# Optimization experiments

Measured on AMD Instinct MI355X. Metric: run time of the kernel, lower is better.

The kernel has to match this reference:

```python
import jax, jax.numpy as jnp
import numpy as np

B, N, D, K, V = 32, 4096, 256, 32, 16


def setup_inputs() -> dict:
    keys = jax.random.split(jax.random.key(0), 6)
    return {
        "rec_scalar_feats": jax.random.normal(keys[0], (B * N, D), jnp.float32),
        "rec_pos": jax.random.normal(keys[1], (B * N, 3), jnp.float32) * 10.0,
        "W_src": jax.random.normal(keys[2], (D, D), jnp.float32) * 0.05,   # nn.Linear weight [out,in]
        "W_dst": jax.random.normal(keys[3], (D, D), jnp.float32) * 0.05,
        "W_kp": jax.random.normal(keys[4], (D * K, D), jnp.float32) * 0.05,  # keypoint_embedding Linear
        "b_kp": jax.random.normal(keys[5], (D * K,), jnp.float32) * 0.01,
        "ln_gamma": jnp.ones((D * K,), jnp.float32),
        "ln_beta": jnp.zeros((D * K,), jnp.float32),
        "batch_size": B,
        "vector_size": V,
    }


def reference(rec_scalar_feats, rec_pos, W_src, W_dst, W_kp, b_kp, ln_gamma, ln_beta, batch_size, vector_size):
    d = rec_scalar_feats.shape[-1]
    b = batch_size
    n = rec_scalar_feats.shape[0] // b
    k = W_kp.shape[0] // d
    h = rec_scalar_feats.reshape(b, n, d)          # rec node scalar features
    pos = rec_pos.reshape(b, n, 3)                 # rec node coordinates (x_0)
    # per-graph mean readout -> keypoint embedding (Linear + SiLU + LayerNorm)
    mean_feats = h.mean(axis=1)                    # [b, d]
    kp = jax.nn.silu(mean_feats @ W_kp.T + b_kp)   # [b, d*k]
    mu = kp.mean(-1, keepdims=True)
    var = kp.var(-1, keepdims=True)
    kp = (kp - mu) * jax.lax.rsqrt(var + 1e-5) * ln_gamma + ln_beta
    kp_scalars_bkd = kp.reshape(b, k, d)
    # edge dot-product attention (num_heads = 1): u_dot_v, exp, segment-normalize == softmax over rec nodes
    ft_src = jnp.einsum("bnd,ed->bne", h, W_src)
    ft_dst = jnp.einsum("bkd,ed->bke", kp_scalars_bkd, W_dst)
    scores = jnp.einsum("bke,bne->bkn", ft_dst, ft_src) / jnp.sqrt(jnp.float32(d))
    w = jax.nn.softmax(scores, axis=-1)            # [b, k, n]
    # scatter-sum of position messages == attention-weighted mean of rec positions
    kp_pos = jnp.einsum("bkn,bnc->bkc", w, pos).reshape(b * k, 3)
    kp_scalars = jnp.zeros((b * k, d), jnp.float32)
    kp_vecs = jnp.zeros((b * k, vector_size, 3), jnp.float32)
    return kp_pos, kp_scalars, kp_vecs
```

## Files before the change

kernel.cpp:

```cpp
#include <hip/hip_runtime.h>
#include <hip/hip_bf16.h>

#define BATCH 32
#define NN 4096
#define KK 32

typedef __attribute__((ext_vector_type(8))) short bf16x8;
typedef __attribute__((ext_vector_type(4))) float f32x4;

#define WS_PART   0
#define WS_WCOMB  131072
#define WS_KP     196608
#define WS_SMP    0
#define WS_G      655360

__device__ __forceinline__ unsigned short f2bf(float x) {
  unsigned int u = __float_as_uint(x);
  u += 0x7fffu + ((u >> 16) & 1u);
  return (unsigned short)(u >> 16);
}

__device__ __forceinline__ unsigned int pk2(float lo, float hi) {
  union { __hip_bfloat162 b; unsigned int u; } c;
  c.b = __float22bfloat162_rn(float2{lo, hi});
  return c.u;
}

__global__ __launch_bounds__(256, 4) void k1_sum_wcomb(
    const float* __restrict__ h, const float* __restrict__ Wsrc,
    const float* __restrict__ Wdst, float* __restrict__ ws,
    float4* __restrict__ out4, int n4) {
  __shared__ float4 sm[256];
  int bk = blockIdx.x, t = threadIdx.x;
  int zi = bk * 256 + t;
  if (zi < n4) out4[zi] = float4{0.f, 0.f, 0.f, 0.f};
  if (bk < 512) {
    int b = bk >> 4, p = bk & 15;
    int c4 = t & 63, rg = t >> 6;
    const float4* hp = (const float4*)h + (((size_t)(b * NN + p * 256)) << 6) + c4;
    float4 acc = {0.f, 0.f, 0.f, 0.f};
    for (int r = rg; r < 256; r += 4) {
      float4 v = hp[(size_t)r << 6];
      acc.x += v.x; acc.y += v.y; acc.z += v.z; acc.w += v.w;
    }
    sm[t] = acc;
    __syncthreads();
    if (t < 64) {
      float4 a = sm[t], b2 = sm[t + 64], c = sm[t + 128], d = sm[t + 192];
      float4 tot = {a.x + b2.x + c.x + d.x, a.y + b2.y + c.y + d.y,
                    a.z + b2.z + c.z + d.z, a.w + b2.w + c.w + d.w};
      ((float4*)(ws + WS_PART))[(size_t)(b * 16 + p) * 64 + t] = tot;
    }
  } else {
    int dp = bk - 512;
    float acc = 0.f;
#pragma unroll 8
    for (int e = 0; e < 256; e++) acc += Wdst[e * 256 + dp] * Wsrc[e * 256 + t];
    ws[WS_WCOMB + dp * 256 + t] = acc;
  }
}

__global__ __launch_bounds__(256, 2) void k2_kp(
    const float* __restrict__ Wkp, const float* __restrict__ bkp,
    float* __restrict__ ws) {
  __shared__ float meanLds[32 * 256];
  int bk = blockIdx.x, t = threadIdx.x;
  for (int idx = t; idx < 8192; idx += 256) {
    int b = idx >> 8, d = idx & 255;
    float s = 0.f;
#pragma unroll
    for (int p = 0; p < 16; p++) s += ws[WS_PART + (size_t)(b * 16 + p) * 256 + d];
    meanLds[idx] = s * (1.0f / NN);
  }
  __syncthreads();
  int j = bk * 128 + (t & 127);
  int bh = (t >> 7) * 16;
  const float4* wrow = (const float4*)(Wkp + (size_t)j * 256);
  float acc[16];
#pragma unroll
  for (int i = 0; i < 16; i++) acc[i] = 0.f;
  for (int d4 = 0; d4 < 64; d4++) {
    float4 wv = wrow[d4];
#pragma unroll
    for (int i = 0; i < 16; i++) {
      float4 m = ((const float4*)meanLds)[(bh + i) * 64 + d4];
      acc[i] += wv.x * m.x + wv.y * m.y + wv.z * m.z + wv.w * m.w;
    }
  }
  float bb = bkp[j];
#pragma unroll
  for (int i = 0; i < 16; i++) {
    float x = acc[i] + bb;
    ws[WS_KP + (size_t)(bh + i) * 8192 + j] = x / (1.0f + __expf(-x));
  }
}

__global__ __launch_bounds__(256, 2) void k3_ln_g(
    const float* __restrict__ ws_in, const float* __restrict__ gamma,
    const float* __restrict__ beta, float* __restrict__ ws) {
  __shared__ float kpl[8192];
  __shared__ float red[8];
  int bx = blockIdx.x, b = blockIdx.y, t = threadIdx.x;
  const float* kp = ws_in + WS_KP + (size_t)b * 8192;
  float4* kpl4 = (float4*)kpl;
  float4 v[8];
  float s = 0.f, sq = 0.f;
#pragma unroll
  for (int i = 0; i < 8; i++) {
    v[i] = ((const float4*)kp)[t + i * 256];
    s += v[i].x + v[i].y + v[i].z + v[i].w;
    sq += v[i].x * v[i].x + v[i].y * v[i].y + v[i].z * v[i].z + v[i].w * v[i].w;
  }
#pragma unroll
  for (int o = 1; o < 64; o <<= 1) { s += __shfl_xor(s, o); sq += __shfl_xor(sq, o); }
  int w = t >> 6, lane = t & 63;
  if (lane == 0) { red[w] = s; red[4 + w] = sq; }
  __syncthreads();
  float S = red[0] + red[1] + red[2] + red[3];
  float SQ = red[4] + red[5] + red[6] + red[7];
  float mu = S * (1.0f / 8192.0f);
  float var = fmaxf(SQ * (1.0f / 8192.0f) - mu * mu, 0.f);
  float rs = rsqrtf(var + 1e-5f);
#pragma unroll
  for (int i = 0; i < 8; i++) {
    float4 g4 = ((const float4*)gamma)[t + i * 256];
    float4 b4 = ((const float4*)beta)[t + i * 256];
    float4 o;
    o.x = ((v[i].x - mu) * rs * g4.x + b4.x) * 0.0625f;
    o.y = ((v[i].y - mu) * rs * g4.y + b4.y) * 0.0625f;
    o.z = ((v[i].z - mu) * rs * g4.z + b4.z) * 0.0625f;
    o.w = ((v[i].w - mu) * rs * g4.w + b4.w) * 0.0625f;
    kpl4[t + i * 256] = o;
  }
  __syncthreads();
  int dc = bx >> 1, kh = bx & 1;
  int d = dc * 64 + lane;
  int k0 = kh * 16 + w * 4;
  const float* wc = ws_in + WS_WCOMB;
  float acc[4] = {0.f, 0.f, 0.f, 0.f};
#pragma unroll 4
  for (int dp4 = 0; dp4 < 64; dp4++) {
    float w0 = wc[(dp4 * 4 + 0) * 256 + d];
    float w1 = wc[(dp4 * 4 + 1) * 256 + d];
    float w2 = wc[(dp4 * 4 + 2) * 256 + d];
    float w3 = wc[(dp4 * 4 + 3) * 256 + d];
#pragma unroll
    for (int i = 0; i < 4; i++) {
      float4 kv = kpl4[(k0 + i) * 64 + dp4];
      acc[i] += kv.x * w0 + kv.y * w1 + kv.z * w2 + kv.w * w3;
    }
  }
  unsigned short* g = (unsigned short*)(ws + WS_G);
#pragma unroll
  for (int i = 0; i < 4; i++) {
    g[(size_t)(b * KK + k0 + i) * 256 + d] = f2bf(acc[i]);
  }
}

__global__ __launch_bounds__(256, 4) void k4_attn(
    const float* __restrict__ h, const float* __restrict__ pos,
    const unsigned short* __restrict__ gbuf, float* __restrict__ ws) {
  __shared__ __align__(16) unsigned short glds[8192];
  const int s = blockIdx.x, b = blockIdx.y, t = threadIdx.x;
  const int lane = t & 63, w = t >> 6;
  const int l15 = lane & 15, l4 = lane >> 4;
  const float LOG2E = 1.4426950408889634f;
  {
    const float4* gsrc = (const float4*)(gbuf + (size_t)b * 8192);
    float4* gdst = (float4*)glds;
    for (int i = t; i < 1024; i += 256) {
      int k = i >> 5, c = i & 31;
      gdst[k * 32 + (c ^ (k & 7))] = gsrc[i];
    }
  }
  __syncthreads();
  const bf16x8* gl = (const bf16x8*)glds;
  const int sw = l15 & 7;

  float m0 = -3.0e38f, m1 = -3.0e38f;
  float L0 = 0.f, L1 = 0.f;
  float P0x = 0.f, P0y = 0.f, P0z = 0.f, P1x = 0.f, P1y = 0.f, P1z = 0.f;

  for (int tile = 0; tile < 2; tile++) {
    int nbase = s * 128 + tile * 64 + w * 16;
    const float4* hp = (const float4*)(h + ((size_t)(b * NN + nbase + l15) << 8));
    int co = l4 * 2;
    f32x4 acc0 = {0.f, 0.f, 0.f, 0.f}, acc1 = {0.f, 0.f, 0.f, 0.f};
#pragma unroll
    for (int kd = 0; kd < 8; kd++) {
      float4 v0 = hp[kd * 8 + co];
      float4 v1 = hp[kd * 8 + co + 1];
      union { unsigned int u[4]; bf16x8 v; } au;
      au.u[0] = pk2(v0.x, v0.y); au.u[1] = pk2(v0.z, v0.w);
      au.u[2] = pk2(v1.x, v1.y); au.u[3] = pk2(v1.z, v1.w);
      int cidx = (kd * 4 + l4) ^ sw;
      bf16x8 g0 = gl[l15 * 32 + cidx];
      bf16x8 g1 = gl[(16 + l15) * 32 + cidx];
      acc0 = __builtin_amdgcn_mfma_f32_16x16x32_bf16(au.v, g0, acc0, 0, 0, 0);
      acc1 = __builtin_amdgcn_mfma_f32_16x16x32_bf16(au.v, g1, acc1, 0, 0, 0);
    }
    float px[4], py[4], pz[4];
#pragma unroll
    for (int j = 0; j < 4; j++) {
      const float* pp = pos + (size_t)(b * NN + nbase + l4 * 4 + j) * 3;
      px[j] = pp[0]; py[j] = pp[1]; pz[j] = pp[2];
    }
    {
      float tm = fmaxf(fmaxf(acc0[0], acc0[1]), fmaxf(acc0[2], acc0[3]));
      tm = fmaxf(tm, __shfl_xor(tm, 16));
      tm = fmaxf(tm, __shfl_xor(tm, 32));
      float mn = fmaxf(m0, tm);
      float corr = exp2f((m0 - mn) * LOG2E);
      float e0 = exp2f((acc0[0] - mn) * LOG2E);
      float e1 = exp2f((acc0[1] - mn) * LOG2E);
      float e2 = exp2f((acc0[2] - mn) * LOG2E);
      float e3 = exp2f((acc0[3] - mn) * LOG2E);
      float se = e0 + e1 + e2 + e3;
      float sx = e0 * px[0] + e1 * px[1] + e2 * px[2] + e3 * px[3];
      float sy = e0 * py[0] + e1 * py[1] + e2 * py[2] + e3 * py[3];
      float sz = e0 * pz[0] + e1 * pz[1] + e2 * pz[2] + e3 * pz[3];
      se += __shfl_xor(se, 16); se += __shfl_xor(se, 32);
      sx += __shfl_xor(sx, 16); sx += __shfl_xor(sx, 32);
      sy += __shfl_xor(sy, 16); sy += __shfl_xor(sy, 32);
      sz += __shfl_xor(sz, 16); sz += __shfl_xor(sz, 32);
      L0 = L0 * corr + se; P0x = P0x * corr + sx;
      P0y = P0y * corr + sy; P0z = P0z * corr + sz; m0 = mn;
    }
    {
      float tm = fmaxf(fmaxf(acc1[0], acc1[1]), fmaxf(acc1[2], acc1[3]));
      tm = fmaxf(tm, __shfl_xor(tm, 16));
      tm = fmaxf(tm, __shfl_xor(tm, 32));
      float mn = fmaxf(m1, tm);
      float corr = exp2f((m1 - mn) * LOG2E);
      float e0 = exp2f((acc1[0] - mn) * LOG2E);
      float e1 = exp2f((acc1[1] - mn) * LOG2E);
      float e2 = exp2f((acc1[2] - mn) * LOG2E);
      float e3 = exp2f((acc1[3] - mn) * LOG2E);
      float se = e0 + e1 + e2 + e3;
      float sx = e0 * px[0] + e1 * px[1] + e2 * px[2] + e3 * px[3];
      float sy = e0 * py[0] + e1 * py[1] + e2 * py[2] + e3 * py[3];
      float sz = e0 * pz[0] + e1 * pz[1] + e2 * pz[2] + e3 * pz[3];
      se += __shfl_xor(se, 16); se += __shfl_xor(se, 32);
      sx += __shfl_xor(sx, 16); sx += __shfl_xor(sx, 32);
      sy += __shfl_xor(sy, 16); sy += __shfl_xor(sy, 32);
      sz += __shfl_xor(sz, 16); sz += __shfl_xor(sz, 32);
      L1 = L1 * corr + se; P1x = P1x * corr + sx;
      P1y = P1y * corr + sy; P1z = P1z * corr + sz; m1 = mn;
    }
  }
  if (lane < 32) {
    int kt = lane >> 4;
    float mv = kt ? m1 : m0;
    float lv = kt ? L1 : L0;
    float pxv = kt ? P1x : P0x;
    float pyv = kt ? P1y : P0y;
    float pzv = kt ? P1z : P0z;
    size_t base = ((size_t)(b * KK + lane)) * 128 + s * 4 + w;
    ws[WS_SMP + base] = mv;
    ws[WS_SMP + 131072 + base] = lv;
    ws[WS_SMP + 262144 + base] = pxv;
    ws[WS_SMP + 393216 + base] = pyv;
    ws[WS_SMP + 524288 + base] = pzv;
  }
}

__global__ void k5_final(const float* __restrict__ smp, float* __restrict__ out) {
  int b = blockIdx.x, t = threadIdx.x;
  const float LOG2E = 1.4426950408889634f;
  int k = t >> 3, sub = t & 7;
  size_t base = ((size_t)(b * KK + k)) * 128;
  float M = -3.0e38f;
#pragma unroll 4
  for (int j = sub; j < 128; j += 8) M = fmaxf(M, smp[base + j]);
#pragma unroll
  for (int o = 1; o < 8; o <<= 1) M = fmaxf(M, __shfl_xor(M, o));
  float L = 0.f, X = 0.f, Y = 0.f, Z = 0.f;
#pragma unroll 4
  for (int j = sub; j < 128; j += 8) {
    float f = exp2f((smp[base + j] - M) * LOG2E);
    L += smp[131072 + base + j] * f;
    X += smp[262144 + base + j] * f;
    Y += smp[393216 + base + j] * f;
    Z += smp[524288 + base + j] * f;
  }
#pragma unroll
  for (int o = 1; o < 8; o <<= 1) {
    L += __shfl_xor(L, o); X += __shfl_xor(X, o);
    Y += __shfl_xor(Y, o); Z += __shfl_xor(Z, o);
  }
  if (sub == 0) {
    float inv = 1.0f / L;
    out[(b * KK + k) * 3 + 0] = X * inv;
    out[(b * KK + k) * 3 + 1] = Y * inv;
    out[(b * KK + k) * 3 + 2] = Z * inv;
  }
}

extern "C" void kernel_launch(void* const* d_in, const int* in_sizes, int n_in,
                              void* d_out, int out_size, void* d_ws, size_t ws_size,
                              hipStream_t stream) {
  const float* h     = (const float*)d_in[0];
  const float* pos   = (const float*)d_in[1];
  const float* Wsrc  = (const float*)d_in[2];
  const float* Wdst  = (const float*)d_in[3];
  const float* Wkp   = (const float*)d_in[4];
  const float* bkp   = (const float*)d_in[5];
  const float* gamma = (const float*)d_in[6];
  const float* beta  = (const float*)d_in[7];
  float* out = (float*)d_out;
  float* ws  = (float*)d_ws;

  k1_sum_wcomb<<<768, 256, 0, stream>>>(h, Wsrc, Wdst, ws, (float4*)d_out,
                                        out_size / 4);
  k2_kp<<<64, 256, 0, stream>>>(Wkp, bkp, ws);
  k3_ln_g<<<dim3(8, BATCH), 256, 0, stream>>>(ws, gamma, beta, ws);
  k4_attn<<<dim3(32, BATCH), 256, 0, stream>>>(h, pos,
                                               (const unsigned short*)(ws + WS_G),
                                               ws);
  k5_final<<<BATCH, 256, 0, stream>>>(ws + WS_SMP, out);
}
```

Before: 102.7 us.

## Fuse first three stages into one cooperative kernel with grid syncs

Merges the column-sum/Wcomb, keypoint-embedding and LayerNorm/projection kernels into a single cooperative launch of 768 blocks, separated by grid-wide barriers. The aim is to remove two kernel-launch boundaries and their gaps. If the cooperative launch fails, it falls back to the three separate kernels. The fused kernel carries 32KB of LDS and a launch bound of 4 blocks per CU, which limits co-residency for the grid-sync requirement. Grid.sync itself also adds overhead, and most blocks sit idle in the later stages.

New measurement: 276.9 us. 2.7x slower.

```diff
diff --git a/kernel.cpp b/kernel.cpp
--- a/kernel.cpp
+++ b/kernel.cpp
@@ -1,5 +1,8 @@
 #include <hip/hip_runtime.h>
 #include <hip/hip_bf16.h>
+#include <hip/hip_cooperative_groups.h>
+
+namespace cg = cooperative_groups;
 
 #define BATCH 32
 #define NN 4096
@@ -26,12 +29,11 @@
   return c.u;
 }
 
-__global__ __launch_bounds__(256, 4) void k1_sum_wcomb(
-    const float* __restrict__ h, const float* __restrict__ Wsrc,
+
+__device__ __forceinline__ void stageA_body(
+    int bk, int t, const float* __restrict__ h, const float* __restrict__ Wsrc,
     const float* __restrict__ Wdst, float* __restrict__ ws,
-    float4* __restrict__ out4, int n4) {
-  __shared__ float4 sm[256];
-  int bk = blockIdx.x, t = threadIdx.x;
+    float4* __restrict__ out4, int n4, float* smem ) {
   int zi = bk * 256 + t;
   if (zi < n4) out4[zi] = float4{0.f, 0.f, 0.f, 0.f};
   if (bk < 512) {
@@ -43,6 +45,7 @@
       float4 v = hp[(size_t)r << 6];
       acc.x += v.x; acc.y += v.y; acc.z += v.z; acc.w += v.w;
     }
+    float4* sm = (float4*)smem;
     sm[t] = acc;
     __syncthreads();
     if (t < 64) {
@@ -60,11 +63,9 @@
   }
 }
 
-__global__ __launch_bounds__(256, 2) void k2_kp(
-    const float* __restrict__ Wkp, const float* __restrict__ bkp,
-    float* __restrict__ ws) {
-  __shared__ float meanLds[32 * 256];
-  int bk = blockIdx.x, t = threadIdx.x;
+__device__ __forceinline__ void stageB_body(
+    int bk, int t, const float* __restrict__ Wkp, const float* __restrict__ bkp,
+    float* __restrict__ ws, float* meanLds ) {
   for (int idx = t; idx < 8192; idx += 256) {
     int b = idx >> 8, d = idx & 255;
     float s = 0.f;
@@ -95,13 +96,11 @@
   }
 }
 
-__global__ __launch_bounds__(256, 2) void k3_ln_g(
-    const float* __restrict__ ws_in, const float* __restrict__ gamma,
-    const float* __restrict__ beta, float* __restrict__ ws) {
-  __shared__ float kpl[8192];
-  __shared__ float red[8];
-  int bx = blockIdx.x, b = blockIdx.y, t = threadIdx.x;
-  const float* kp = ws_in + WS_KP + (size_t)b * 8192;
+__device__ __forceinline__ void stageC_body(
+    int bx, int b, int t, const float* __restrict__ gamma,
+    const float* __restrict__ beta, float* __restrict__ ws,
+    float* kpl , float* red ) {
+  const float* kp = ws + WS_KP + (size_t)b * 8192;
   float4* kpl4 = (float4*)kpl;
   float4 v[8];
   float s = 0.f, sq = 0.f;
@@ -136,7 +135,7 @@
   int dc = bx >> 1, kh = bx & 1;
   int d = dc * 64 + lane;
   int k0 = kh * 16 + w * 4;
-  const float* wc = ws_in + WS_WCOMB;
+  const float* wc = ws + WS_WCOMB;
   float acc[4] = {0.f, 0.f, 0.f, 0.f};
 #pragma unroll 4
   for (int dp4 = 0; dp4 < 64; dp4++) {
@@ -155,6 +154,47 @@
   for (int i = 0; i < 4; i++) {
     g[(size_t)(b * KK + k0 + i) * 256 + d] = f2bf(acc[i]);
   }
+}
+
+__global__ __launch_bounds__(256, 4) void kA_fused(
+    const float* __restrict__ h, const float* __restrict__ Wsrc,
+    const float* __restrict__ Wdst, const float* __restrict__ Wkp,
+    const float* __restrict__ bkp, const float* __restrict__ gamma,
+    const float* __restrict__ beta, float* __restrict__ ws,
+    float4* __restrict__ out4, int n4) {
+  cg::grid_group grid = cg::this_grid();
+  __shared__ __align__(16) float smem[8192];
+  __shared__ float red[8];
+  int bk = blockIdx.x, t = threadIdx.x;
+
+  stageA_body(bk, t, h, Wsrc, Wdst, ws, out4, n4, smem);
+  grid.sync();
+  if (bk < 64) stageB_body(bk, t, Wkp, bkp, ws, smem);
+  grid.sync();
+  if (bk < 256) stageC_body(bk & 7, bk >> 3, t, gamma, beta, ws, smem, red);
+}
+
+__global__ __launch_bounds__(256, 4) void k1_sep(
+    const float* __restrict__ h, const float* __restrict__ Wsrc,
+    const float* __restrict__ Wdst, float* __restrict__ ws,
+    float4* __restrict__ out4, int n4) {
+  __shared__ __align__(16) float smem[1024];
+  stageA_body(blockIdx.x, threadIdx.x, h, Wsrc, Wdst, ws, out4, n4, smem);
+}
+
+__global__ __launch_bounds__(256, 2) void k2_sep(
+    const float* __restrict__ Wkp, const float* __restrict__ bkp,
+    float* __restrict__ ws) {
+  __shared__ __align__(16) float smem[8192];
+  stageB_body(blockIdx.x, threadIdx.x, Wkp, bkp, ws, smem);
+}
+
+__global__ __launch_bounds__(256, 2) void k3_sep(
+    const float* __restrict__ gamma, const float* __restrict__ beta,
+    float* __restrict__ ws) {
+  __shared__ __align__(16) float smem[8192];
+  __shared__ float red[8];
+  stageC_body(blockIdx.x, blockIdx.y, threadIdx.x, gamma, beta, ws, smem, red);
 }
 
 __global__ __launch_bounds__(256, 4) void k4_attn(
@@ -309,11 +349,19 @@
   const float* beta  = (const float*)d_in[7];
   float* out = (float*)d_out;
   float* ws  = (float*)d_ws;
-
-  k1_sum_wcomb<<<768, 256, 0, stream>>>(h, Wsrc, Wdst, ws, (float4*)d_out,
-                                        out_size / 4);
-  k2_kp<<<64, 256, 0, stream>>>(Wkp, bkp, ws);
-  k3_ln_g<<<dim3(8, BATCH), 256, 0, stream>>>(ws, gamma, beta, ws);
+  float4* out4 = (float4*)d_out;
+  int n4 = out_size / 4;
+
+  void* args[] = {(void*)&h, (void*)&Wsrc, (void*)&Wdst, (void*)&Wkp,
+                  (void*)&bkp, (void*)&gamma, (void*)&beta, (void*)&ws,
+                  (void*)&out4, (void*)&n4};
+  hipError_t err = hipLaunchCooperativeKernel((const void*)kA_fused, dim3(768),
+                                              dim3(256), args, 0, stream);
+  if (err != hipSuccess) {
+    k1_sep<<<768, 256, 0, stream>>>(h, Wsrc, Wdst, ws, out4, n4);
+    k2_sep<<<64, 256, 0, stream>>>(Wkp, bkp, ws);
+    k3_sep<<<dim3(8, BATCH), 256, 0, stream>>>(gamma, beta, ws);
+  }
   k4_attn<<<dim3(32, BATCH), 256, 0, stream>>>(h, pos,
                                                (const unsigned short*)(ws + WS_G),
                                                ws);
```
